# Kernel tuning notes

Hardware: AMD Instinct MI355X
Metric: run time of the kernel (lower is better)

## Reference

```python
import jax, jax.numpy as jnp
import numpy as np

B, S, D, H, DK, F = 4, 2048, 1024, 16, 64, 4096


def layer_norm(x, g, b, eps=1e-5):
    mu = jnp.mean(x, axis=-1, keepdims=True)
    var = jnp.var(x, axis=-1, keepdims=True)
    return (x - mu) * jax.lax.rsqrt(var + eps) * g + b


def setup_inputs() -> dict:
    key = jax.random.key(0)
    ks = jax.random.split(key, 16)
    s = 0.02
    return {
        "src": jax.random.normal(ks[0], (B, S, D), jnp.float32),
        # per-head q/k/v projections stacked over heads: (H, D, DK)
        "Wq": jax.random.normal(ks[1], (H, D, DK), jnp.float32) * s,
        "bq": jnp.zeros((H, DK), jnp.float32),
        "Wk": jax.random.normal(ks[2], (H, D, DK), jnp.float32) * s,
        "bk": jnp.zeros((H, DK), jnp.float32),
        "Wv": jax.random.normal(ks[3], (H, D, DK), jnp.float32) * s,
        "bv": jnp.zeros((H, DK), jnp.float32),
        "Wo": jax.random.normal(ks[4], (H * DK, D), jnp.float32) * s,
        "bo": jnp.zeros((D,), jnp.float32),
        "ln1_g": jnp.ones((D,), jnp.float32),
        "ln1_b": jnp.zeros((D,), jnp.float32),
        "W1": jax.random.normal(ks[5], (D, F), jnp.float32) * s,
        "b1": jnp.zeros((F,), jnp.float32),
        "W2": jax.random.normal(ks[6], (F, D), jnp.float32) * s,
        "b2": jnp.zeros((D,), jnp.float32),
        "ln2_g": jnp.ones((D,), jnp.float32),
        "ln2_b": jnp.zeros((D,), jnp.float32),
    }


def reference(src, Wq, bq, Wk, bk, Wv, bv, Wo, bo, ln1_g, ln1_b, W1, b1, W2, b2, ln2_g, ln2_b):
    # --- multi-head attention (all heads batched via einsum) ---
    q = jnp.einsum("bsd,hdk->bhsk", src, Wq) + bq[None, :, None, :]
    k = jnp.einsum("bsd,hdk->bhsk", src, Wk) + bk[None, :, None, :]
    v = jnp.einsum("bsd,hdk->bhsk", src, Wv) + bv[None, :, None, :]
    scale = jnp.sqrt(jnp.asarray(DK, q.dtype))
    scores = jnp.einsum("bhqk,bhsk->bhqs", q, k) / scale  # [B,H,S,S]
    p = jax.nn.softmax(scores, axis=-1)
    ctx = jnp.einsum("bhqs,bhsk->bhqk", p, v)             # [B,H,S,DK]
    ctx = ctx.transpose(0, 2, 1, 3).reshape(src.shape[0], src.shape[1], H * DK)
    attn_out = ctx @ Wo + bo
    x = layer_norm(src + attn_out, ln1_g, ln1_b)
    # --- feed-forward ---
    ff = jax.nn.relu(x @ W1 + b1) @ W2 + b2
    return layer_norm(x + ff, ln2_g, ln2_b)
```

## Files before the change

### kernel.cpp

```cpp
#include <hip/hip_runtime.h>
#include <hip/hip_bf16.h>
#include <cstddef>
#include <cstdint>

typedef __bf16 bf16;
typedef __bf16 bf16x4 __attribute__((ext_vector_type(4)));
typedef __bf16 bf16x8 __attribute__((ext_vector_type(8)));
typedef float f32x4 __attribute__((ext_vector_type(4)));
typedef float f32x16 __attribute__((ext_vector_type(16)));
typedef unsigned int u32x4 __attribute__((ext_vector_type(4)));

#define GLD_LDS16(g, l) __builtin_amdgcn_global_load_lds( \
    (const __attribute__((address_space(1))) void*)(g),   \
    (__attribute__((address_space(3))) void*)(l), 16, 0, 0)

#define SBAR __builtin_amdgcn_s_barrier()
#define SCHED0 __builtin_amdgcn_sched_barrier(0)
#define VMW(n) asm volatile("s_waitcnt vmcnt(" #n ")" ::: "memory")

static __device__ inline unsigned int cvtpk(float lo, float hi) {
  unsigned int r;
  asm("v_cvt_pk_bf16_f32 %0, %1, %2" : "=v"(r) : "v"(lo), "v"(hi));
  return r;
}
static __device__ inline void plswap(unsigned int& a, unsigned int& b) {
  asm("v_permlane32_swap_b32 %0, %1" : "+v"(a), "+v"(b));
}
static __device__ inline float fexp2(float x) {
#if __has_builtin(__builtin_amdgcn_exp2f)
  return __builtin_amdgcn_exp2f(x);
#else
  float r; asm("v_exp_f32 %0, %1" : "=v"(r) : "v"(x)); return r;
#endif
}
static __device__ inline float tsum16(const float* e) {
  float s0 = e[0] + e[1], s1 = e[2] + e[3], s2 = e[4] + e[5], s3 = e[6] + e[7];
  float s4 = e[8] + e[9], s5 = e[10] + e[11], s6 = e[12] + e[13], s7 = e[14] + e[15];
  return ((s0 + s1) + (s2 + s3)) + ((s4 + s5) + (s6 + s7));
}

__global__ void __launch_bounds__(256)
k_cast(const float* __restrict__ in, bf16* __restrict__ out) {
  int gid = blockIdx.x * 256 + threadIdx.x;
  f32x4 a = ((const f32x4*)in)[gid * 2];
  f32x4 b = ((const f32x4*)in)[gid * 2 + 1];
  bf16x8 o;
#pragma unroll
  for (int i = 0; i < 4; ++i) { o[i] = (bf16)a[i]; o[i + 4] = (bf16)b[i]; }
  ((bf16x8*)out)[gid] = o;
}

__global__ void __launch_bounds__(256)
k_transpose_t(const float* __restrict__ in, bf16* __restrict__ out, int R, int C) {
  __shared__ float tile[64][68];
  const int nct = C >> 6;
  const int bc = blockIdx.x % nct, br = blockIdx.x / nct;
  const int r0 = br << 6, c0 = bc << 6;
  const int t = threadIdx.x;
  const int tr = t >> 4, tc4 = (t & 15) << 2;
#pragma unroll
  for (int i = 0; i < 4; ++i)
    *(f32x4*)&tile[i * 16 + tr][tc4] =
        *(const f32x4*)&in[(size_t)(r0 + i * 16 + tr) * C + c0 + tc4];
  __syncthreads();
  const int c = t >> 2, rch = (t & 3) << 4;
  bf16 ob[16];
#pragma unroll
  for (int j = 0; j < 16; ++j) ob[j] = (bf16)tile[rch + j][c];
  bf16* dst = out + (size_t)(c0 + c) * R + r0 + rch;
  *(bf16x8*)&dst[0] = *(bf16x8*)&ob[0];
  *(bf16x8*)&dst[8] = *(bf16x8*)&ob[8];
}

__global__ void __launch_bounds__(256)
k_reorder_qkv_t(const float* __restrict__ Wq, const float* __restrict__ Wk,
                const float* __restrict__ Wv, bf16* __restrict__ WqkvT) {
  __shared__ float tile[64][68];
  const int bid = blockIdx.x;
  const int sub = bid >> 4, tl = bid & 15;
  const int proj = sub >> 4, h = sub & 15;
  const float* W = (proj == 0) ? Wq : (proj == 1) ? Wk : Wv;
  const float* src = W + (size_t)h * 65536;
  const int r0 = tl << 6;
  const int t = threadIdx.x, tr = t >> 4, tc4 = (t & 15) << 2;
#pragma unroll
  for (int i = 0; i < 4; ++i)
    *(f32x4*)&tile[i * 16 + tr][tc4] =
        *(const f32x4*)&src[(size_t)(r0 + i * 16 + tr) * 64 + tc4];
  __syncthreads();
  const int c = t >> 2, rch = (t & 3) << 4;
  bf16 ob[16];
#pragma unroll
  for (int j = 0; j < 16; ++j) ob[j] = (bf16)tile[rch + j][c];
  bf16* dst = WqkvT + ((size_t)(proj * 1024 + h * 64 + c)) * 1024 + r0 + rch;
  *(bf16x8*)&dst[0] = *(bf16x8*)&ob[0];
  *(bf16x8*)&dst[8] = *(bf16x8*)&ob[8];
}

__global__ void __launch_bounds__(256)
k_bias_qkv(const float* __restrict__ bq, const float* __restrict__ bk,
           const float* __restrict__ bv, float* __restrict__ bqkv) {
  int n = blockIdx.x * 256 + threadIdx.x;
  int proj = n >> 10, wi = n & 1023;
  const float* bb = (proj == 0) ? bq : (proj == 1) ? bk : bv;
  bqkv[n] = bb[wi];
}

template <int MODE, int NREP>
__global__ void __launch_bounds__(512, 1)
k_gemm4(const bf16* __restrict__ A, const bf16* __restrict__ Bt,
        const float* __restrict__ bias, void* __restrict__ outp,
        int M, int N, int K, int klen, int splitk,
        bf16* __restrict__ qb, bf16* __restrict__ kb, bf16* __restrict__ vb) {
  constexpr int BN = 128 * NREP;
  constexpr int BROWS = 64 * NREP;
  __shared__ __align__(16) bf16 Asl[4][8192];
  __shared__ __align__(16) bf16 Bsl[4][BROWS * 64];

  const int tid = threadIdx.x;
  const int lane = tid & 63, wave = tid >> 6;
  const int l16 = lane & 15, lq = lane >> 4;
  const int qwm = wave >> 2, qwn = wave & 3;

  const int tiles = gridDim.x / splitk;
  const int twg = blockIdx.x % tiles;
  const int sk = blockIdx.x / tiles;
  const int k0 = sk * klen;
  const int mtiles = M >> 8;
  const int tile_m = (twg % mtiles) << 8;
  const int tile_n = (twg / mtiles) * BN;

  const bf16* Abase = A + (size_t)tile_m * K + k0;
  const bf16* Bbase = Bt + (size_t)tile_n * K + k0;

  const int crow = tid >> 3;
  const int ccol = ((tid & 7) ^ (crow & 7)) << 3;

  auto stageA = [&](int T, int h, int slot) {
    const bf16* s_ = Abase + (size_t)(h * 128 + crow) * K + T * 64 + ccol;
    GLD_LDS16(s_, &Asl[slot][tid * 8]);
    GLD_LDS16(s_ + (size_t)64 * K, &Asl[slot][tid * 8 + 4096]);
  };
  auto stageB = [&](int T, int h, int slot) {
    const bf16* s_ = Bbase + (size_t)(h * BROWS + crow) * K + T * 64 + ccol;
    GLD_LDS16(s_, &Bsl[slot][tid * 8]);
    if (NREP == 2) GLD_LDS16(s_ + (size_t)64 * K, &Bsl[slot][tid * 8 + 4096]);
  };

  const int xk = l16 & 7;
  const int swz0 = (lq ^ xk) * 16;
  const int swz1 = ((4 | lq) ^ xk) * 16;
  const int arow_b = (qwm * 64 + l16) * 128;
  const int brow_b = (qwn * 16 * NREP + l16) * 128;

  bf16x8 af[4][2];
  bf16x8 bb[2][NREP][2];
  f32x4 acc[2][2][4][NREP] = {};

  auto dsA = [&](int slot) {
    const char* Ab = (const char*)&Asl[slot][0] + arow_b;
#pragma unroll
    for (int mi = 0; mi < 4; ++mi) {
      af[mi][0] = *(const bf16x8*)(Ab + mi * 2048 + swz0);
      af[mi][1] = *(const bf16x8*)(Ab + mi * 2048 + swz1);
    }
  };
  auto dsB2 = [&](int slot0, int slot1) {
    const char* B0 = (const char*)&Bsl[slot0][0] + brow_b;
    const char* B1 = (const char*)&Bsl[slot1][0] + brow_b;
#pragma unroll
    for (int ni = 0; ni < NREP; ++ni) {
      bb[0][ni][0] = *(const bf16x8*)(B0 + ni * 2048 + swz0);
      bb[0][ni][1] = *(const bf16x8*)(B0 + ni * 2048 + swz1);
      bb[1][ni][0] = *(const bf16x8*)(B1 + ni * 2048 + swz0);
      bb[1][ni][1] = *(const bf16x8*)(B1 + ni * 2048 + swz1);
    }
  };
  auto MF2 = [&](int mh) {
    __builtin_amdgcn_s_setprio(1);
#pragma unroll
    for (int nh = 0; nh < 2; ++nh)
#pragma unroll
      for (int mi = 0; mi < 4; ++mi)
#pragma unroll
        for (int ni = 0; ni < NREP; ++ni)
#pragma unroll
          for (int p = 0; p < 2; ++p)
            acc[mh][nh][mi][ni] = __builtin_amdgcn_mfma_f32_16x16x32_bf16(
                af[mi][p], bb[nh][ni][p], acc[mh][nh][mi][ni], 0, 0, 0);
    __builtin_amdgcn_s_setprio(0);
  };

  const int NT = klen >> 6;
  const int NI = NT >> 1;

  stageA(0, 0, 0); stageA(0, 1, 1); stageB(0, 0, 0); stageB(0, 1, 1);
  stageA(1, 0, 2); stageB(1, 0, 2); stageB(1, 1, 3);
  SCHED0;
  if (NREP == 2) { VMW(6); } else { VMW(4); }
  SBAR;

  for (int i = 0; i < NI; ++i) {
    const int t2 = 2 * i + 2, t3 = 2 * i + 3;
    const bool tv = (t2 < NT);
    dsA(0); dsB2(0, 1);
    stageA(2 * i + 1, 1, 3);
    SBAR; MF2(0); SBAR;
    dsA(1);
    if (tv) { stageA(t2, 0, 0); stageB(t2, 0, 0); }
    SCHED0;
    if (!tv) { VMW(0); }
    else if (NREP == 2) { VMW(4); } else { VMW(3); }
    SBAR; MF2(1); SBAR;
    dsA(2); dsB2(2, 3);
    if (tv) { stageA(t2, 1, 1); stageB(t2, 1, 1); }
    SBAR; MF2(0); SBAR;
    dsA(3);
    if (tv) {
      stageA(t3, 0, 2); stageB(t3, 0, 2); stageB(t3, 1, 3);
      SCHED0;
      if (NREP == 2) { VMW(6); } else { VMW(4); }
    }
    SBAR; MF2(1); SBAR;
  }

  float* psplit = (MODE == 3) ? ((float*)outp + (size_t)sk * M * N) : nullptr;
#pragma unroll
  for (int mh = 0; mh < 2; ++mh)
#pragma unroll
    for (int nh = 0; nh < 2; ++nh)
#pragma unroll
      for (int mi = 0; mi < 4; ++mi)
#pragma unroll
        for (int ni = 0; ni < NREP; ++ni) {
          const int gn = tile_n + nh * (BN / 2) + qwn * 16 * NREP + ni * 16 + l16;
          const float bv = (MODE == 3) ? 0.f : bias[gn];
          f32x4 v = acc[mh][nh][mi][ni];
          const int gm0 = tile_m + mh * 128 + qwm * 64 + mi * 16 + lq * 4;
          if (MODE == 0) {
            int proj = gn >> 10, wi = gn & 1023;
            int h = wi >> 6, dk = wi & 63;
            int b = gm0 >> 11, sdx = gm0 & 2047;
            size_t bhs = (size_t)((b << 4) + h);
            if (proj == 0) {
#pragma unroll
              for (int i2 = 0; i2 < 4; ++i2)
                qb[(bhs * 2048 + sdx + i2) * 64 + dk] = (bf16)((v[i2] + bv) * 0.18033688f);
            } else if (proj == 1) {
#pragma unroll
              for (int i2 = 0; i2 < 4; ++i2)
                kb[(bhs * 2048 + sdx + i2) * 64 + dk] = (bf16)(v[i2] + bv);
            } else {
              bf16x4 pk;
#pragma unroll
              for (int i2 = 0; i2 < 4; ++i2) pk[i2] = (bf16)(v[i2] + bv);
              *(bf16x4*)&vb[(bhs * 64 + dk) * 2048 + sdx] = pk;
            }
          } else if (MODE == 1) {
#pragma unroll
            for (int i2 = 0; i2 < 4; ++i2)
              ((bf16*)outp)[(size_t)(gm0 + i2) * N + gn] = (bf16)(v[i2] + bv);
          } else if (MODE == 2) {
#pragma unroll
            for (int i2 = 0; i2 < 4; ++i2)
              ((bf16*)outp)[(size_t)(gm0 + i2) * N + gn] = (bf16)fmaxf(v[i2] + bv, 0.f);
          } else {
#pragma unroll
            for (int i2 = 0; i2 < 4; ++i2)
              psplit[(size_t)(gm0 + i2) * N + gn] = v[i2];
          }
        }
}

__global__ void __launch_bounds__(256, 2)
k_attn(const bf16* __restrict__ qb, const bf16* __restrict__ kb,
       const bf16* __restrict__ vb, bf16* __restrict__ ctx) {
  __shared__ __align__(16) bf16 KsL[3][4096];
  __shared__ __align__(16) bf16 VsL[3][4096];

  const int bid = blockIdx.x;
  const int wg = (bid & 7) * 64 + (bid >> 3);
  const int bh = wg >> 3, qt = wg & 7;

  const bf16* Qp  = qb + (size_t)bh * 131072 + (size_t)qt * 16384;
  const bf16* Kbh = kb + (size_t)bh * 131072;
  const bf16* Vbh = vb + (size_t)bh * 131072;

  const int tid = threadIdx.x, wave = tid >> 6, lane = tid & 63;
  const int l31 = lane & 31, hi = lane >> 5;

  bf16x8 qfA[4], qfB[4];
  {
    const bf16* qra = Qp + (size_t)(wave * 64 + l31) * 64 + hi * 8;
    const bf16* qrb = qra + 32 * 64;
#pragma unroll
    for (int kd = 0; kd < 4; ++kd) {
      qfA[kd] = *(const bf16x8*)(qra + kd * 16);
      qfB[kd] = *(const bf16x8*)(qrb + kd * 16);
    }
  }

  const int c0 = tid, c1 = tid + 256;
  const int sw0 = ((c0 ^ (c0 >> 3)) & 7) * 8, rw0 = c0 >> 3;
  const int sw1 = ((c1 ^ (c1 >> 3)) & 7) * 8, rw1 = c1 >> 3;
  const int kof0 = rw0 * 64 + sw0, kof1 = rw1 * 64 + sw1;
  const int vof0 = rw0 * 2048 + sw0, vof1 = rw1 * 2048 + sw1;

  const int xr = (hi << 4) ^ ((l31 & 7) << 4);
  const int rb = l31 * 128 + xr;

  f32x16 oA[2] = {}, oB[2] = {};
  float lA = 0.f, lB = 0.f;

#define STAGE_KV(buf, s0)                                             \
  do {                                                                \
    GLD_LDS16(Kbh + (size_t)(s0) * 64 + kof0, &KsL[buf][c0 * 8]);     \
    GLD_LDS16(Kbh + (size_t)(s0) * 64 + kof1, &KsL[buf][c1 * 8]);     \
    GLD_LDS16(Vbh + (s0) + vof0, &VsL[buf][c0 * 8]);                  \
    GLD_LDS16(Vbh + (s0) + vof1, &VsL[buf][c1 * 8]);                  \
  } while (0)

  STAGE_KV(0, 0);
  STAGE_KV(1, 64);

  int cur = 0;
  for (int kt = 0; kt < 32; ++kt) {
    SCHED0;
    if (kt == 31) { VMW(0); }
    else          { VMW(4); }
    __builtin_amdgcn_s_barrier();
    SCHED0;

    if (kt < 30) {
      int nx = cur + 2; if (nx >= 3) nx -= 3;
      STAGE_KV(nx, (kt + 2) * 64);
    }

    const char* Kc = (const char*)&KsL[cur][0];
    const char* Vc = (const char*)&VsL[cur][0];

    bf16x8 paA[4], paB[4];
#pragma unroll
    for (int st = 0; st < 2; ++st) {
      f32x16 sA = {}, sB = {};
      __builtin_amdgcn_s_setprio(1);
#pragma unroll
      for (int kd = 0; kd < 4; ++kd) {
        bf16x8 a = *(const bf16x8*)(Kc + st * 4096 + (rb ^ (kd << 5)));
        sA = __builtin_amdgcn_mfma_f32_32x32x16_bf16(a, qfA[kd], sA, 0, 0, 0);
        sB = __builtin_amdgcn_mfma_f32_32x32x16_bf16(a, qfB[kd], sB, 0, 0, 0);
      }
      __builtin_amdgcn_s_setprio(0);

      float eA[16], eB[16];
#pragma unroll
      for (int i = 0; i < 16; ++i) {
        eA[i] = fexp2(sA[i]);
        eB[i] = fexp2(sB[i]);
      }
      lA += tsum16(eA);
      lB += tsum16(eB);
      unsigned int qdA[4][2], qdB[4][2];
#pragma unroll
      for (int g = 0; g < 4; ++g)
#pragma unroll
        for (int w = 0; w < 2; ++w) {
          qdA[g][w] = cvtpk(eA[g * 4 + w * 2], eA[g * 4 + w * 2 + 1]);
          qdB[g][w] = cvtpk(eB[g * 4 + w * 2], eB[g * 4 + w * 2 + 1]);
        }
#pragma unroll
      for (int a2 = 0; a2 < 2; ++a2) {
        unsigned int x0 = qdA[2 * a2][0], y0 = qdA[2 * a2 + 1][0];
        unsigned int x1 = qdA[2 * a2][1], y1 = qdA[2 * a2 + 1][1];
        plswap(x0, y0); plswap(x1, y1);
        u32x4 fA = {x0, x1, y0, y1};
        paA[st * 2 + a2] = __builtin_bit_cast(bf16x8, fA);
        unsigned int u0 = qdB[2 * a2][0], v0 = qdB[2 * a2 + 1][0];
        unsigned int u1 = qdB[2 * a2][1], v1 = qdB[2 * a2 + 1][1];
        plswap(u0, v0); plswap(u1, v1);
        u32x4 fB = {u0, u1, v0, v1};
        paB[st * 2 + a2] = __builtin_bit_cast(bf16x8, fB);
      }
    }

    __builtin_amdgcn_s_setprio(1);
#pragma unroll
    for (int nd = 0; nd < 2; ++nd)
#pragma unroll
      for (int ks = 0; ks < 4; ++ks) {
        bf16x8 vf = *(const bf16x8*)(Vc + nd * 4096 + (rb ^ (ks << 5)));
        oA[nd] = __builtin_amdgcn_mfma_f32_32x32x16_bf16(paA[ks], vf, oA[nd], 0, 0, 0);
        oB[nd] = __builtin_amdgcn_mfma_f32_32x32x16_bf16(paB[ks], vf, oB[nd], 0, 0, 0);
      }
    __builtin_amdgcn_s_setprio(0);

    if (++cur == 3) cur = 0;
  }
#undef STAGE_KV

  const float ltA = lA + __shfl_xor(lA, 32);
  const float ltB = lB + __shfl_xor(lB, 32);
  const float ivA = 1.f / ltA;
  const float ivB = 1.f / ltB;

  const int b = bh >> 4, h = bh & 15;
  const size_t rowbase = (size_t)(b * 2048 + qt * 256 + wave * 64);
#pragma unroll
  for (int r = 0; r < 16; ++r) {
    const int qr = (r & 3) + 8 * (r >> 2) + 4 * hi;
    const float dA = __shfl(ivA, qr);
    const float dB = __shfl(ivB, qr);
#pragma unroll
    for (int nd = 0; nd < 2; ++nd) {
      const int dk = nd * 32 + l31;
      ctx[(rowbase + qr) * 1024 + h * 64 + dk]      = (bf16)(oA[nd][r] * dA);
      ctx[(rowbase + 32 + qr) * 1024 + h * 64 + dk] = (bf16)(oB[nd][r] * dB);
    }
  }
}

template <typename RT, typename DT, typename OT>
__global__ void __launch_bounds__(256)
k_ln(const RT* __restrict__ resid, const DT* __restrict__ delta,
     const float* __restrict__ g, const float* __restrict__ bta,
     OT* __restrict__ out) {
  const int row = blockIdx.x, tid = threadIdx.x;
  const int wave = tid >> 6, lane = tid & 63;
  __shared__ float rs_[4], rs2_[4];
  const RT* r = resid + (size_t)row * 1024;
  const DT* d = delta + (size_t)row * 1024;
  OT* o = out + (size_t)row * 1024;
  float x[4], s = 0.f, s2 = 0.f;
#pragma unroll
  for (int j = 0; j < 4; ++j) {
    int idx = tid + j * 256;
    float v = (float)r[idx] + (float)d[idx];
    x[j] = v; s += v; s2 += v * v;
  }
#pragma unroll
  for (int m = 32; m >= 1; m >>= 1) { s += __shfl_xor(s, m); s2 += __shfl_xor(s2, m); }
  if (lane == 0) { rs_[wave] = s; rs2_[wave] = s2; }
  __syncthreads();
  float ts = rs_[0] + rs_[1] + rs_[2] + rs_[3];
  float ts2 = rs2_[0] + rs2_[1] + rs2_[2] + rs2_[3];
  float mean = ts * (1.f / 1024.f);
  float var = ts2 * (1.f / 1024.f) - mean * mean;
  float rstd = rsqrtf(var + 1e-5f);
#pragma unroll
  for (int j = 0; j < 4; ++j) {
    int idx = tid + j * 256;
    o[idx] = (OT)((x[j] - mean) * rstd * g[idx] + bta[idx]);
  }
}

__global__ void __launch_bounds__(256)
k_ln_sk(const bf16* __restrict__ x1r, const float* __restrict__ p0,
        const float* __restrict__ p1, const float* __restrict__ bias,
        const float* __restrict__ g, const float* __restrict__ bta,
        float* __restrict__ out) {
  const int row = blockIdx.x, tid = threadIdx.x;
  const int wave = tid >> 6, lane = tid & 63;
  __shared__ float rs_[4], rs2_[4];
  const bf16* r = x1r + (size_t)row * 1024;
  const float* a = p0 + (size_t)row * 1024;
  const float* b = p1 + (size_t)row * 1024;
  float* o = out + (size_t)row * 1024;
  float x[4], s = 0.f, s2 = 0.f;
#pragma unroll
  for (int j = 0; j < 4; ++j) {
    int idx = tid + j * 256;
    float v = (float)r[idx] + a[idx] + b[idx] + bias[idx];
    x[j] = v; s += v; s2 += v * v;
  }
#pragma unroll
  for (int m = 32; m >= 1; m >>= 1) { s += __shfl_xor(s, m); s2 += __shfl_xor(s2, m); }
  if (lane == 0) { rs_[wave] = s; rs2_[wave] = s2; }
  __syncthreads();
  float ts = rs_[0] + rs_[1] + rs_[2] + rs_[3];
  float ts2 = rs2_[0] + rs2_[1] + rs2_[2] + rs2_[3];
  float mean = ts * (1.f / 1024.f);
  float var = ts2 * (1.f / 1024.f) - mean * mean;
  float rstd = rsqrtf(var + 1e-5f);
#pragma unroll
  for (int j = 0; j < 4; ++j) {
    int idx = tid + j * 256;
    o[idx] = (x[j] - mean) * rstd * g[idx] + bta[idx];
  }
}

extern "C" void kernel_launch(void* const* d_in, const int* in_sizes, int n_in,
                              void* d_out, int out_size, void* d_ws, size_t ws_size,
                              hipStream_t stream) {
  const float* src  = (const float*)d_in[0];
  const float* Wq   = (const float*)d_in[1];
  const float* bq   = (const float*)d_in[2];
  const float* Wk   = (const float*)d_in[3];
  const float* bk   = (const float*)d_in[4];
  const float* Wv   = (const float*)d_in[5];
  const float* bv   = (const float*)d_in[6];
  const float* Wo   = (const float*)d_in[7];
  const float* bo   = (const float*)d_in[8];
  const float* ln1g = (const float*)d_in[9];
  const float* ln1b = (const float*)d_in[10];
  const float* W1   = (const float*)d_in[11];
  const float* b1   = (const float*)d_in[12];
  const float* W2   = (const float*)d_in[13];
  const float* b2   = (const float*)d_in[14];
  const float* ln2g = (const float*)d_in[15];
  const float* ln2b = (const float*)d_in[16];

  char* p = (char*)d_ws;
  bf16*  WqkvT = (bf16*)p;  p += (size_t)3072 * 1024 * 2;
  float* bqkv  = (float*)p; p += 16384;
  bf16*  WoT   = (bf16*)p;  p += (size_t)1024 * 1024 * 2;
  bf16*  W1T   = (bf16*)p;  p += (size_t)4096 * 1024 * 2;
  bf16*  W2T   = (bf16*)p;  p += (size_t)1024 * 4096 * 2;
  bf16*  srcb  = (bf16*)p;  p += (size_t)8388608 * 2;
  bf16*  qbuf  = (bf16*)p;  p += (size_t)8388608 * 2;
  bf16*  kbuf  = (bf16*)p;  p += (size_t)8388608 * 2;
  bf16*  vbuf  = (bf16*)p;  p += (size_t)8388608 * 2;
  bf16*  ctx   = (bf16*)p;  p += (size_t)8388608 * 2;
  bf16*  x1    = (bf16*)p;  p += (size_t)8388608 * 2;
  bf16*  ff1   = (bf16*)p;  p += (size_t)8192 * 4096 * 2;
  bf16*  tmp   = qbuf;
  float* pk0   = (float*)srcb;

  k_cast<<<4096, 256, 0, stream>>>(src, srcb);
  k_reorder_qkv_t<<<768, 256, 0, stream>>>(Wq, Wk, Wv, WqkvT);
  k_bias_qkv<<<12, 256, 0, stream>>>(bq, bk, bv, bqkv);
  k_transpose_t<<<256, 256, 0, stream>>>(Wo, WoT, 1024, 1024);
  k_transpose_t<<<1024, 256, 0, stream>>>(W1, W1T, 1024, 4096);
  k_transpose_t<<<1024, 256, 0, stream>>>(W2, W2T, 4096, 1024);

  k_gemm4<0, 1><<<768, 512, 0, stream>>>(srcb, WqkvT, bqkv, nullptr,
                                         8192, 3072, 1024, 1024, 1, qbuf, kbuf, vbuf);
  k_attn<<<512, 256, 0, stream>>>(qbuf, kbuf, vbuf, ctx);
  k_gemm4<1, 1><<<256, 512, 0, stream>>>(ctx, WoT, bo, tmp,
                                         8192, 1024, 1024, 1024, 1, nullptr, nullptr, nullptr);
  k_ln<float, bf16, bf16><<<8192, 256, 0, stream>>>(src, tmp, ln1g, ln1b, x1);
  k_gemm4<2, 2><<<512, 512, 0, stream>>>(x1, W1T, b1, ff1,
                                         8192, 4096, 1024, 1024, 1, nullptr, nullptr, nullptr);
  k_gemm4<3, 2><<<256, 512, 0, stream>>>(ff1, W2T, nullptr, pk0,
                                         8192, 1024, 4096, 2048, 2, nullptr, nullptr, nullptr);
  k_ln_sk<<<8192, 256, 0, stream>>>(x1, pk0, pk0 + (size_t)8192 * 1024, b2,
                                    ln2g, ln2b, (float*)d_out);
}
```

Measured before the change: 482.2 us.

## Split attention across 8 waves, use NREP=2 for QKV GEMM, finer vmcnt waits

Attention blocks grow to 512 threads, and each wave handles 32 query rows instead of 64. This halves the per-wave accumulator and register footprint and spreads the K/V staging over more threads. The QKV projection GEMM switches to the NREP=2 variant with half as many blocks. The GEMM main loop adds finer-grained vmcnt waits before each MFMA phase. k_ln_sk is made templated with no behaviour change. The trade-offs are more waves competing per CU, Q-tile reuse across a wave dropping from two tiles to one, and waits that could stall earlier.

New measurement: 495.8 us. +2.8%, slower.

```diff
diff --git a/kernel.cpp b/kernel.cpp
--- a/kernel.cpp
+++ b/kernel.cpp
@@ -205,15 +205,20 @@
     const bool tv = (t2 < NT);
     dsA(0); dsB2(0, 1);
     stageA(2 * i + 1, 1, 3);
+    SCHED0;
+    if (NREP == 2) { VMW(10); } else { VMW(7); }
     SBAR; MF2(0); SBAR;
     dsA(1);
     if (tv) { stageA(t2, 0, 0); stageB(t2, 0, 0); }
     SCHED0;
-    if (!tv) { VMW(0); }
-    else if (NREP == 2) { VMW(4); } else { VMW(3); }
+    if (!tv) { VMW(2); }
+    else if (NREP == 2) { VMW(6); } else { VMW(5); }
     SBAR; MF2(1); SBAR;
     dsA(2); dsB2(2, 3);
     if (tv) { stageA(t2, 1, 1); stageB(t2, 1, 1); }
+    SCHED0;
+    if (!tv) { VMW(0); }
+    else if (NREP == 2) { VMW(8); } else { VMW(6); }
     SBAR; MF2(0); SBAR;
     dsA(3);
     if (tv) {
@@ -272,7 +277,7 @@
         }
 }
 
-__global__ void __launch_bounds__(256, 2)
+__global__ void __launch_bounds__(512, 4)
 k_attn(const bf16* __restrict__ qb, const bf16* __restrict__ kb,
        const bf16* __restrict__ vb, bf16* __restrict__ ctx) {
   __shared__ __align__(16) bf16 KsL[3][4096];
@@ -289,35 +294,28 @@
   const int tid = threadIdx.x, wave = tid >> 6, lane = tid & 63;
   const int l31 = lane & 31, hi = lane >> 5;
 
-  bf16x8 qfA[4], qfB[4];
+  bf16x8 qf[4];
   {
-    const bf16* qra = Qp + (size_t)(wave * 64 + l31) * 64 + hi * 8;
-    const bf16* qrb = qra + 32 * 64;
-#pragma unroll
-    for (int kd = 0; kd < 4; ++kd) {
-      qfA[kd] = *(const bf16x8*)(qra + kd * 16);
-      qfB[kd] = *(const bf16x8*)(qrb + kd * 16);
-    }
-  }
-
-  const int c0 = tid, c1 = tid + 256;
+    const bf16* qra = Qp + (size_t)(wave * 32 + l31) * 64 + hi * 8;
+#pragma unroll
+    for (int kd = 0; kd < 4; ++kd) qf[kd] = *(const bf16x8*)(qra + kd * 16);
+  }
+
+  const int c0 = tid;
   const int sw0 = ((c0 ^ (c0 >> 3)) & 7) * 8, rw0 = c0 >> 3;
-  const int sw1 = ((c1 ^ (c1 >> 3)) & 7) * 8, rw1 = c1 >> 3;
-  const int kof0 = rw0 * 64 + sw0, kof1 = rw1 * 64 + sw1;
-  const int vof0 = rw0 * 2048 + sw0, vof1 = rw1 * 2048 + sw1;
+  const int kof0 = rw0 * 64 + sw0;
+  const int vof0 = rw0 * 2048 + sw0;
 
   const int xr = (hi << 4) ^ ((l31 & 7) << 4);
   const int rb = l31 * 128 + xr;
 
-  f32x16 oA[2] = {}, oB[2] = {};
-  float lA = 0.f, lB = 0.f;
+  f32x16 oA[2] = {};
+  float lA = 0.f;
 
 #define STAGE_KV(buf, s0)                                             \
   do {                                                                \
     GLD_LDS16(Kbh + (size_t)(s0) * 64 + kof0, &KsL[buf][c0 * 8]);     \
-    GLD_LDS16(Kbh + (size_t)(s0) * 64 + kof1, &KsL[buf][c1 * 8]);     \
     GLD_LDS16(Vbh + (s0) + vof0, &VsL[buf][c0 * 8]);                  \
-    GLD_LDS16(Vbh + (s0) + vof1, &VsL[buf][c1 * 8]);                  \
   } while (0)
 
   STAGE_KV(0, 0);
@@ -327,7 +325,7 @@
   for (int kt = 0; kt < 32; ++kt) {
     SCHED0;
     if (kt == 31) { VMW(0); }
-    else          { VMW(4); }
+    else          { VMW(2); }
     __builtin_amdgcn_s_barrier();
     SCHED0;
 
@@ -339,35 +337,28 @@
     const char* Kc = (const char*)&KsL[cur][0];
     const char* Vc = (const char*)&VsL[cur][0];
 
-    bf16x8 paA[4], paB[4];
+    bf16x8 paA[4];
 #pragma unroll
     for (int st = 0; st < 2; ++st) {
-      f32x16 sA = {}, sB = {};
+      f32x16 sA = {};
       __builtin_amdgcn_s_setprio(1);
 #pragma unroll
       for (int kd = 0; kd < 4; ++kd) {
         bf16x8 a = *(const bf16x8*)(Kc + st * 4096 + (rb ^ (kd << 5)));
-        sA = __builtin_amdgcn_mfma_f32_32x32x16_bf16(a, qfA[kd], sA, 0, 0, 0);
-        sB = __builtin_amdgcn_mfma_f32_32x32x16_bf16(a, qfB[kd], sB, 0, 0, 0);
+        sA = __builtin_amdgcn_mfma_f32_32x32x16_bf16(a, qf[kd], sA, 0, 0, 0);
       }
       __builtin_amdgcn_s_setprio(0);
 
-      float eA[16], eB[16];
-#pragma unroll
-      for (int i = 0; i < 16; ++i) {
-        eA[i] = fexp2(sA[i]);
-        eB[i] = fexp2(sB[i]);
-      }
+      float eA[16];
+#pragma unroll
+      for (int i = 0; i < 16; ++i) eA[i] = fexp2(sA[i]);
       lA += tsum16(eA);
-      lB += tsum16(eB);
-      unsigned int qdA[4][2], qdB[4][2];
+      unsigned int qdA[4][2];
 #pragma unroll
       for (int g = 0; g < 4; ++g)
 #pragma unroll
-        for (int w = 0; w < 2; ++w) {
+        for (int w = 0; w < 2; ++w)
           qdA[g][w] = cvtpk(eA[g * 4 + w * 2], eA[g * 4 + w * 2 + 1]);
-          qdB[g][w] = cvtpk(eB[g * 4 + w * 2], eB[g * 4 + w * 2 + 1]);
-        }
 #pragma unroll
       for (int a2 = 0; a2 < 2; ++a2) {
         unsigned int x0 = qdA[2 * a2][0], y0 = qdA[2 * a2 + 1][0];
@@ -375,11 +366,6 @@
         plswap(x0, y0); plswap(x1, y1);
         u32x4 fA = {x0, x1, y0, y1};
         paA[st * 2 + a2] = __builtin_bit_cast(bf16x8, fA);
-        unsigned int u0 = qdB[2 * a2][0], v0 = qdB[2 * a2 + 1][0];
-        unsigned int u1 = qdB[2 * a2][1], v1 = qdB[2 * a2 + 1][1];
-        plswap(u0, v0); plswap(u1, v1);
-        u32x4 fB = {u0, u1, v0, v1};
-        paB[st * 2 + a2] = __builtin_bit_cast(bf16x8, fB);
       }
     }
 
@@ -390,7 +376,6 @@
       for (int ks = 0; ks < 4; ++ks) {
         bf16x8 vf = *(const bf16x8*)(Vc + nd * 4096 + (rb ^ (ks << 5)));
         oA[nd] = __builtin_amdgcn_mfma_f32_32x32x16_bf16(paA[ks], vf, oA[nd], 0, 0, 0);
-        oB[nd] = __builtin_amdgcn_mfma_f32_32x32x16_bf16(paB[ks], vf, oB[nd], 0, 0, 0);
       }
     __builtin_amdgcn_s_setprio(0);
 
@@ -399,22 +384,18 @@
 #undef STAGE_KV
 
   const float ltA = lA + __shfl_xor(lA, 32);
-  const float ltB = lB + __shfl_xor(lB, 32);
   const float ivA = 1.f / ltA;
-  const float ivB = 1.f / ltB;
 
   const int b = bh >> 4, h = bh & 15;
-  const size_t rowbase = (size_t)(b * 2048 + qt * 256 + wave * 64);
+  const size_t rowbase = (size_t)(b * 2048 + qt * 256 + wave * 32);
 #pragma unroll
   for (int r = 0; r < 16; ++r) {
     const int qr = (r & 3) + 8 * (r >> 2) + 4 * hi;
     const float dA = __shfl(ivA, qr);
-    const float dB = __shfl(ivB, qr);
 #pragma unroll
     for (int nd = 0; nd < 2; ++nd) {
       const int dk = nd * 32 + l31;
-      ctx[(rowbase + qr) * 1024 + h * 64 + dk]      = (bf16)(oA[nd][r] * dA);
-      ctx[(rowbase + 32 + qr) * 1024 + h * 64 + dk] = (bf16)(oB[nd][r] * dB);
+      ctx[(rowbase + qr) * 1024 + h * 64 + dk] = (bf16)(oA[nd][r] * dA);
     }
   }
 }
@@ -453,18 +434,19 @@
   }
 }
 
+template <typename RT, typename OT>
 __global__ void __launch_bounds__(256)
-k_ln_sk(const bf16* __restrict__ x1r, const float* __restrict__ p0,
+k_ln_sk(const RT* __restrict__ resid, const float* __restrict__ p0,
         const float* __restrict__ p1, const float* __restrict__ bias,
         const float* __restrict__ g, const float* __restrict__ bta,
-        float* __restrict__ out) {
+        OT* __restrict__ out) {
   const int row = blockIdx.x, tid = threadIdx.x;
   const int wave = tid >> 6, lane = tid & 63;
   __shared__ float rs_[4], rs2_[4];
-  const bf16* r = x1r + (size_t)row * 1024;
+  const RT* r = resid + (size_t)row * 1024;
   const float* a = p0 + (size_t)row * 1024;
   const float* b = p1 + (size_t)row * 1024;
-  float* o = out + (size_t)row * 1024;
+  OT* o = out + (size_t)row * 1024;
   float x[4], s = 0.f, s2 = 0.f;
 #pragma unroll
   for (int j = 0; j < 4; ++j) {
@@ -484,7 +466,7 @@
 #pragma unroll
   for (int j = 0; j < 4; ++j) {
     int idx = tid + j * 256;
-    o[idx] = (x[j] - mean) * rstd * g[idx] + bta[idx];
+    o[idx] = (OT)((x[j] - mean) * rstd * g[idx] + bta[idx]);
   }
 }
 
@@ -524,6 +506,7 @@
   bf16*  ff1   = (bf16*)p;  p += (size_t)8192 * 4096 * 2;
   bf16*  tmp   = qbuf;
   float* pk0   = (float*)srcb;
+  float* pk1   = pk0 + (size_t)8192 * 1024;
 
   k_cast<<<4096, 256, 0, stream>>>(src, srcb);
   k_reorder_qkv_t<<<768, 256, 0, stream>>>(Wq, Wk, Wv, WqkvT);
@@ -532,9 +515,9 @@
   k_transpose_t<<<1024, 256, 0, stream>>>(W1, W1T, 1024, 4096);
   k_transpose_t<<<1024, 256, 0, stream>>>(W2, W2T, 4096, 1024);
 
-  k_gemm4<0, 1><<<768, 512, 0, stream>>>(srcb, WqkvT, bqkv, nullptr,
+  k_gemm4<0, 2><<<384, 512, 0, stream>>>(srcb, WqkvT, bqkv, nullptr,
                                          8192, 3072, 1024, 1024, 1, qbuf, kbuf, vbuf);
-  k_attn<<<512, 256, 0, stream>>>(qbuf, kbuf, vbuf, ctx);
+  k_attn<<<512, 512, 0, stream>>>(qbuf, kbuf, vbuf, ctx);
   k_gemm4<1, 1><<<256, 512, 0, stream>>>(ctx, WoT, bo, tmp,
                                          8192, 1024, 1024, 1024, 1, nullptr, nullptr, nullptr);
   k_ln<float, bf16, bf16><<<8192, 256, 0, stream>>>(src, tmp, ln1g, ln1b, x1);
@@ -542,6 +525,6 @@
                                          8192, 4096, 1024, 1024, 1, nullptr, nullptr, nullptr);
   k_gemm4<3, 2><<<256, 512, 0, stream>>>(ff1, W2T, nullptr, pk0,
                                          8192, 1024, 4096, 2048, 2, nullptr, nullptr, nullptr);
-  k_ln_sk<<<8192, 256, 0, stream>>>(x1, pk0, pk0 + (size_t)8192 * 1024, b2,
-                                    ln2g, ln2b, (float*)d_out);
-}
+  k_ln_sk<bf16, float><<<8192, 256, 0, stream>>>(x1, pk0, pk1, b2,
+                                                 ln2g, ln2b, (float*)d_out);
+}
```
